# Kernel optimization log

Measured on AMD Instinct MI355X. Metric: run time of the kernel, lower is better.

Reference implementation:

```python
import jax, jax.numpy as jnp
import numpy as np

N_NODES = 1024
CHANNELS = [1, 64, 128]
DENSE = [196608, 256]
SAMPLE_NUMBER = 50


def _glorot(key, shape):
    fan_in, fan_out = shape[0], shape[-1]
    s = jnp.sqrt(6.0 / (fan_in + fan_out))
    return jax.random.uniform(key, shape, jnp.float32, -s, s)


def setup_inputs() -> dict:
    key = jax.random.key(0)
    ks = jax.random.split(key, 20)
    T, B = 16, 64
    inp = {
        "xs_seq": jax.random.normal(ks[0], (T, B, N_NODES, CHANNELS[0]), jnp.float32),
        "adj": jax.random.uniform(ks[1], (N_NODES, N_NODES), jnp.float32) / N_NODES,
    }
    # GCGRU params per layer: gates z, r, candidate n over concat([x, h])
    ki = 2
    for li in range(len(CHANNELS) - 1):
        cin, cout = CHANNELS[li], CHANNELS[li + 1]
        for g in ("z", "r", "n"):
            inp[f"W{g}{li}"] = _glorot(ks[ki], (cin + cout, cout)); ki += 1
            inp[f"b{g}{li}"] = jnp.zeros((cout,), jnp.float32)
    inp["W_mu"] = _glorot(ks[ki], (DENSE[0], DENSE[1])); ki += 1
    inp["b_mu"] = jnp.zeros((DENSE[1],), jnp.float32)
    inp["W_lv"] = _glorot(ks[ki], (DENSE[0], DENSE[1])); ki += 1
    inp["b_lv"] = jnp.zeros((DENSE[1],), jnp.float32)
    return inp


def _gcgru(xs, adj, Wz, bz, Wr, br, Wn, bn, cout):
    # xs: [T, B, N, cin]; graph-conv GRU over time via scan
    T, B, N, _ = xs.shape
    h0 = jnp.zeros((B, N, cout), xs.dtype)

    def gconv(a, x, W, b):  # adj @ x @ W + b
        return jnp.einsum("ij,bjc,cd->bid", a, x, W) + b

    def step(h, x):
        xh = jnp.concatenate([x, h], axis=-1)
        z = jax.nn.sigmoid(gconv(adj, xh, Wz, bz))
        r = jax.nn.sigmoid(gconv(adj, xh, Wr, br))
        xrh = jnp.concatenate([x, r * h], axis=-1)
        n = jnp.tanh(gconv(adj, xrh, Wn, bn))
        h_new = (1.0 - z) * h + z * n
        return h_new, h_new

    _, hs = jax.lax.scan(step, h0, xs)
    return hs  # [T, B, N, cout]


def _forward(xs_seq, adj, Wz0, bz0, Wr0, br0, Wn0, bn0,
             Wz1, bz1, Wr1, br1, Wn1, bn1, W_mu, b_mu, W_lv, b_lv, eps):
    h1 = _gcgru(xs_seq, adj, Wz0, bz0, Wr0, br0, Wn0, bn0, CHANNELS[1])
    h2 = _gcgru(h1, adj, Wz1, bz1, Wr1, br1, Wn1, bn1, CHANNELS[2])
    xs = jnp.concatenate([h1[-1], h2[-1]], axis=2)  # [B, N, C1+C2]
    B = xs.shape[0]
    xs = xs.reshape(B, -1)  # [B, N*(C1+C2)]
    mu = jax.nn.sigmoid(xs @ W_mu + b_mu)
    logvar = jax.nn.sigmoid(xs @ W_lv + b_lv)
    std = jnp.exp(0.5 * logvar)
    z = mu + eps * std
    return z, mu, logvar


def reference(xs_seq, adj, Wz0, bz0, Wr0, br0, Wn0, bn0,
              Wz1, bz1, Wr1, br1, Wn1, bn1, W_mu, b_mu, W_lv, b_lv):
    B = xs_seq.shape[1]
    ekey = jax.random.fold_in(jax.random.key(0), 1234)
    eps = jax.random.normal(ekey, (SAMPLE_NUMBER, B, DENSE[1]), jnp.float32).mean(0)
    return _forward(xs_seq, adj, Wz0, bz0, Wr0, br0, Wn0, bn0,
                    Wz1, bz1, Wr1, br1, Wn1, bn1, W_mu, b_mu, W_lv, b_lv, eps)
```

## Files before the change

kernel.cpp:

```cpp
#include <hip/hip_runtime.h>
#include <math.h>

#define EPS_MODE 0

typedef unsigned short u16;
typedef short bf16x8 __attribute__((ext_vector_type(8)));
typedef float f32x4 __attribute__((ext_vector_type(4)));
typedef u16 u16x4 __attribute__((ext_vector_type(4)));
typedef u16 u16x8 __attribute__((ext_vector_type(8)));

static constexpr int T = 16;
static constexpr size_t MF = 1u << 20;

__device__ __forceinline__ u16 f2bf(float f) {
  unsigned u = __float_as_uint(f);
  unsigned r = (u + 0x7fffu + ((u >> 16) & 1u)) >> 16;
  return (u16)r;
}
__device__ __forceinline__ float bf2f(u16 h) {
  return __uint_as_float(((unsigned)h) << 16);
}
__device__ __forceinline__ void gload16(const void* g, void* l) {
  __builtin_amdgcn_global_load_lds(
      (const __attribute__((address_space(1))) void*)g,
      (__attribute__((address_space(3))) void*)l, 16, 0, 0);
}

__global__ __launch_bounds__(256) void cast_bf16(const float* __restrict__ in,
                                                 u16* __restrict__ out, int n) {
  int i = (blockIdx.x * 256 + threadIdx.x) * 4;
  if (i < n) {
    float4 v = *reinterpret_cast<const float4*>(&in[i]);
    out[i + 0] = f2bf(v.x); out[i + 1] = f2bf(v.y);
    out[i + 2] = f2bf(v.z); out[i + 3] = f2bf(v.w);
  }
}

__global__ __launch_bounds__(256) void prep_wt(const float* __restrict__ Wz0, const float* __restrict__ Wr0,
                                               const float* __restrict__ Wn0, const float* __restrict__ Wz1,
                                               const float* __restrict__ Wr1, const float* __restrict__ Wn1,
                                               u16* __restrict__ WzrT0, u16* __restrict__ WnT0,
                                               u16* __restrict__ WzrT1, u16* __restrict__ WnT1) {
  int seg = blockIdx.y;
  int idx = blockIdx.x * 256 + threadIdx.x;
  if (seg == 0) {
    if (idx < 128 * 64) {
      int j = idx >> 6, k = idx & 63;
      float v = (j < 64) ? Wz0[(k + 1) * 64 + j] : Wr0[(k + 1) * 64 + (j - 64)];
      WzrT0[idx] = f2bf(v);
    }
  } else if (seg == 1) {
    if (idx < 64 * 64) {
      int j = idx >> 6, k = idx & 63;
      WnT0[idx] = f2bf(Wn0[(k + 1) * 64 + j]);
    }
  } else if (seg == 2) {
    if (idx < 256 * 192) {
      int j = idx / 192, k = idx % 192;
      float v = (j < 128) ? Wz1[k * 128 + j] : Wr1[k * 128 + (j - 128)];
      WzrT1[idx] = f2bf(v);
    }
  } else {
    if (idx < 128 * 192) {
      int j = idx / 192, k = idx % 192;
      WnT1[idx] = f2bf(Wn1[k * 128 + j]);
    }
  }
}

template <int EPI, int LOGC>
__global__ __launch_bounds__(256) void adj_mfma(const u16* __restrict__ A,
                                                const u16* __restrict__ BT,
                                                void* __restrict__ OUT) {
  __shared__ __align__(16) char lds[32768];
  int tid = threadIdx.x;
  int w = tid >> 6, lane = tid & 63;
  int row0 = blockIdx.y * 128, col0 = blockIdx.x * 128;
  int wm = w >> 1, wn = w & 1;
  f32x4 acc[4][4] = {};
  for (int k0 = 0; k0 < 1024; k0 += 64) {
#pragma unroll
    for (int q = 0; q < 4; ++q) {
      int row = q * 32 + w * 8 + (lane >> 3);
      gload16(A + (size_t)(row0 + row) * 1024 + k0 + (lane & 7) * 8,
              lds + q * 4096 + w * 1024);
    }
#pragma unroll
    for (int q = 0; q < 4; ++q) {
      int row = q * 32 + w * 8 + (lane >> 3);
      gload16(BT + (size_t)(col0 + row) * 1024 + k0 + (lane & 7) * 8,
              lds + 16384 + q * 4096 + w * 1024);
    }
    __syncthreads();
#pragma unroll
    for (int kk = 0; kk < 2; ++kk) {
      bf16x8 a[4], bb[4];
#pragma unroll
      for (int m = 0; m < 4; ++m)
        a[m] = *(const bf16x8*)(lds + (wm * 64 + m * 16 + (lane & 15)) * 128 + kk * 64 + (lane >> 4) * 16);
#pragma unroll
      for (int n = 0; n < 4; ++n)
        bb[n] = *(const bf16x8*)(lds + 16384 + (wn * 64 + n * 16 + (lane & 15)) * 128 + kk * 64 + (lane >> 4) * 16);
#pragma unroll
      for (int m = 0; m < 4; ++m)
#pragma unroll
        for (int n = 0; n < 4; ++n)
          acc[m][n] = __builtin_amdgcn_mfma_f32_16x16x32_bf16(a[m], bb[n], acc[m][n], 0, 0, 0);
    }
    __syncthreads();
  }
  if (EPI == 1) {
    float* O = (float*)OUT;
#pragma unroll
    for (int m = 0; m < 4; ++m)
#pragma unroll
      for (int n = 0; n < 4; ++n) {
        int col = col0 + wn * 64 + n * 16 + (lane & 15);
        int t = col >> 6, bbx = col & 63;
        int row = row0 + wm * 64 + m * 16 + ((lane >> 4) << 2);
        *(float4*)&O[((size_t)t << 16) + ((size_t)bbx << 10) + row] = *(float4*)&acc[m][n];
      }
  } else {
    u16* O = (u16*)OUT;
    constexpr int C = 1 << LOGC;
#pragma unroll
    for (int m = 0; m < 4; ++m)
#pragma unroll
      for (int n = 0; n < 4; ++n) {
        int col = col0 + wn * 64 + n * 16 + (lane & 15);
        int bbx = col >> LOGC, c = col & (C - 1);
#pragma unroll
        for (int j = 0; j < 4; ++j) {
          int row = row0 + wm * 64 + m * 16 + ((lane >> 4) << 2) + j;
          O[(((size_t)bbx << 10) + row) * C + c] = f2bf(acc[m][n][j]);
        }
      }
  }
}

template <int C, int RK1>
__global__ __launch_bounds__(256) void adj_ngate(
    const u16* __restrict__ A, const u16* __restrict__ BT,
    const u16* __restrict__ WnT, const float* __restrict__ bias,
    const float* __restrict__ axv, const float* __restrict__ wx,
    const u16* __restrict__ AH1, const u16* __restrict__ zT,
    u16* __restrict__ hT) {
  constexpr int LOGC = (C == 64) ? 6 : 7;
  constexpr int KW = (C == 64) ? 64 : 192;
  constexpr int KKAN = C / 32;
  __shared__ __align__(16) char lds[136 * 128 * 2];
  int tid = threadIdx.x;
  int w = tid >> 6, lane = tid & 63;
  int row0 = blockIdx.y * 128, col0 = blockIdx.x * 128;
  int wm = w >> 1, wn = w & 1;
  f32x4 acc[4][4] = {};
  for (int k0 = 0; k0 < 1024; k0 += 64) {
#pragma unroll
    for (int q = 0; q < 4; ++q) {
      int row = q * 32 + w * 8 + (lane >> 3);
      gload16(A + (size_t)(row0 + row) * 1024 + k0 + (lane & 7) * 8,
              lds + q * 4096 + w * 1024);
    }
#pragma unroll
    for (int q = 0; q < 4; ++q) {
      int row = q * 32 + w * 8 + (lane >> 3);
      gload16(BT + (size_t)(col0 + row) * 1024 + k0 + (lane & 7) * 8,
              lds + 16384 + q * 4096 + w * 1024);
    }
    __syncthreads();
#pragma unroll
    for (int kk = 0; kk < 2; ++kk) {
      bf16x8 a[4], bb[4];
#pragma unroll
      for (int m = 0; m < 4; ++m)
        a[m] = *(const bf16x8*)(lds + (wm * 64 + m * 16 + (lane & 15)) * 128 + kk * 64 + (lane >> 4) * 16);
#pragma unroll
      for (int n = 0; n < 4; ++n)
        bb[n] = *(const bf16x8*)(lds + 16384 + (wn * 64 + n * 16 + (lane & 15)) * 128 + kk * 64 + (lane >> 4) * 16);
#pragma unroll
      for (int m = 0; m < 4; ++m)
#pragma unroll
        for (int n = 0; n < 4; ++n)
          acc[m][n] = __builtin_amdgcn_mfma_f32_16x16x32_bf16(a[m], bb[n], acc[m][n], 0, 0, 0);
    }
    __syncthreads();
  }
  u16* ANt = (u16*)lds;
#pragma unroll
  for (int m = 0; m < 4; ++m)
#pragma unroll
    for (int n = 0; n < 4; ++n) {
      int cl = wn * 64 + n * 16 + (lane & 15);
      int rl = wm * 64 + m * 16 + ((lane >> 4) << 2);
#pragma unroll
      for (int j = 0; j < 4; ++j)
        ANt[(rl + j) * 136 + cl] = f2bf(acc[m][n][j]);
    }
  __syncthreads();
  int arow0 = (w >> 1) * 64;
  int half = w & 1;
  int b0 = col0 >> LOGC;
  int out0 = (C == 64) ? 0 : half * 64;
  int kbase = (C == 64) ? half * 64 : 0;
  int b_eff = (C == 64) ? (b0 + half) : b0;
  constexpr int WOFF = (C == 64) ? 0 : 64;
  f32x4 acc2[4][4] = {};
#pragma unroll
  for (int kk = 0; kk < KKAN; ++kk) {
    bf16x8 a[4], bb[4];
    int ka = kbase + kk * 32 + (lane >> 4) * 8;
#pragma unroll
    for (int m = 0; m < 4; ++m)
      a[m] = *(const bf16x8*)&ANt[(arow0 + m * 16 + (lane & 15)) * 136 + ka];
#pragma unroll
    for (int n = 0; n < 4; ++n)
      bb[n] = *(const bf16x8*)&WnT[(size_t)(out0 + n * 16 + (lane & 15)) * KW + WOFF + kk * 32 + (lane >> 4) * 8];
#pragma unroll
    for (int m = 0; m < 4; ++m)
#pragma unroll
      for (int n = 0; n < 4; ++n)
        acc2[m][n] = __builtin_amdgcn_mfma_f32_16x16x32_bf16(a[m], bb[n], acc2[m][n], 0, 0, 0);
  }
  if (C == 128) {
#pragma unroll
    for (int kk = 0; kk < 2; ++kk) {
      bf16x8 a[4], bb[4];
#pragma unroll
      for (int m = 0; m < 4; ++m)
        a[m] = *(const bf16x8*)&AH1[(((size_t)b0 << 10) + row0 + arow0 + m * 16 + (lane & 15)) * 64 + kk * 32 + (lane >> 4) * 8];
#pragma unroll
      for (int n = 0; n < 4; ++n)
        bb[n] = *(const bf16x8*)&WnT[(size_t)(out0 + n * 16 + (lane & 15)) * 192 + kk * 32 + (lane >> 4) * 8];
#pragma unroll
      for (int m = 0; m < 4; ++m)
#pragma unroll
        for (int n = 0; n < 4; ++n)
          acc2[m][n] = __builtin_amdgcn_mfma_f32_16x16x32_bf16(a[m], bb[n], acc2[m][n], 0, 0, 0);
    }
  }
#pragma unroll
  for (int m = 0; m < 4; ++m) {
    float ax4[4];
    if (RK1) {
      float4 v = *(const float4*)&axv[((size_t)b_eff << 10) + row0 + arow0 + m * 16 + ((lane >> 4) << 2)];
      ax4[0] = v.x; ax4[1] = v.y; ax4[2] = v.z; ax4[3] = v.w;
    }
#pragma unroll
    for (int n = 0; n < 4; ++n) {
      int cp = out0 + n * 16 + (lane & 15);
      int grow = arow0 + m * 16 + ((lane >> 4) << 2);
      size_t idx = (((size_t)b_eff << LOGC) + cp) * 1024 + row0 + grow;
      u16x4 zv = *(const u16x4*)&zT[idx];
      u16x4 hv = *(const u16x4*)&hT[idx];
      u16x4 pk;
#pragma unroll
      for (int j = 0; j < 4; ++j) {
        float g = acc2[m][n][j] + bias[cp];
        if (RK1) g += ax4[j] * wx[cp];
        float nv = tanhf(g);
        float z = bf2f(zv[j]), ho = bf2f(hv[j]);
        pk[j] = f2bf((1.f - z) * ho + z * nv);
      }
      *(u16x4*)&hT[idx] = pk;
    }
  }
}

template <int WM, int WN, int C, int NK1, int NK, int RK1>
__global__ __launch_bounds__(256) void gate_zr(
    const u16* __restrict__ A1, const u16* __restrict__ A2,
    const u16* __restrict__ WT, const float* __restrict__ bz,
    const float* __restrict__ br, const float* __restrict__ axv,
    const float* __restrict__ wxz, const float* __restrict__ wxr,
    const u16* __restrict__ hT, u16* __restrict__ zTo, u16* __restrict__ rhTo) {
  constexpr int MT = WM * 64, NT = WN * 64, K = NK * 64;
  constexpr int NB = 1024 / MT;
  __shared__ __align__(16) char lds[MT * 128 + NT * 128];
  int tid = threadIdx.x;
  int w = tid >> 6, lane = tid & 63;
  int by = blockIdx.x;
  int b = by / NB, n0 = (by % NB) * MT;
  size_t row0 = ((size_t)b << 10) + n0;
  int wm = w / WN, wn = w % WN;
  f32x4 acc[4][4] = {};
  for (int s = 0; s < NK; ++s) {
    const u16* As; int astr, koff;
    if (s < NK1) { As = A1; astr = 64; koff = s * 64; }
    else         { As = A2; astr = 128; koff = (s - NK1) * 64; }
#pragma unroll
    for (int q = 0; q < MT / 32; ++q) {
      int row = q * 32 + w * 8 + (lane >> 3);
      gload16(As + (row0 + row) * astr + koff + (lane & 7) * 8,
              lds + q * 4096 + w * 1024);
    }
#pragma unroll
    for (int q = 0; q < NT / 32; ++q) {
      int row = q * 32 + w * 8 + (lane >> 3);
      gload16(WT + (size_t)row * K + s * 64 + (lane & 7) * 8,
              lds + MT * 128 + q * 4096 + w * 1024);
    }
    __syncthreads();
#pragma unroll
    for (int kk = 0; kk < 2; ++kk) {
      bf16x8 a[4], bb[4];
#pragma unroll
      for (int m = 0; m < 4; ++m)
        a[m] = *(const bf16x8*)(lds + (wm * 64 + m * 16 + (lane & 15)) * 128 + kk * 64 + (lane >> 4) * 16);
#pragma unroll
      for (int n = 0; n < 4; ++n)
        bb[n] = *(const bf16x8*)(lds + MT * 128 + (wn * 64 + n * 16 + (lane & 15)) * 128 + kk * 64 + (lane >> 4) * 16);
#pragma unroll
      for (int m = 0; m < 4; ++m)
#pragma unroll
        for (int n = 0; n < 4; ++n)
          acc[m][n] = __builtin_amdgcn_mfma_f32_16x16x32_bf16(a[m], bb[n], acc[m][n], 0, 0, 0);
    }
    __syncthreads();
  }
#pragma unroll
  for (int m = 0; m < 4; ++m) {
    float ax4[4];
    if (RK1) {
      float4 v = *(const float4*)&axv[row0 + wm * 64 + m * 16 + ((lane >> 4) << 2)];
      ax4[0] = v.x; ax4[1] = v.y; ax4[2] = v.z; ax4[3] = v.w;
    }
#pragma unroll
    for (int n = 0; n < 4; ++n) {
      int cp = wn * 64 + n * 16 + (lane & 15);
      bool iz = cp < C;
      int c = iz ? cp : cp - C;
      int rl = wm * 64 + m * 16 + ((lane >> 4) << 2);
      size_t idx = (((size_t)b * C + c) << 10) + n0 + rl;
      u16x4 hv;
      if (!iz) hv = *(const u16x4*)&hT[idx];
      u16x4 pk;
#pragma unroll
      for (int j = 0; j < 4; ++j) {
        float g = acc[m][n][j] + (iz ? bz : br)[c];
        if (RK1) g += ax4[j] * (iz ? wxz : wxr)[c];
        float sg = 1.f / (1.f + expf(-g));
        pk[j] = iz ? f2bf(sg) : f2bf(sg * bf2f(hv[j]));
      }
      *(u16x4*)&(iz ? zTo : rhTo)[idx] = pk;
    }
  }
}

__global__ __launch_bounds__(256) void dense_gemm(const u16* __restrict__ h1T,
                                                  const u16* __restrict__ h2T,
                                                  const float* __restrict__ Wmu,
                                                  const float* __restrict__ Wlv,
                                                  float* __restrict__ P) {
  int ch = blockIdx.x, mat = blockIdx.y;
  const float* W = mat ? Wlv : Wmu;
  __shared__ float As[64][36];
  __shared__ float Ws[32][260];
  int tid = threadIdx.x;
  int k0 = ch * 512;
  bool is1 = ch < 128;
  const u16* hs = is1 ? h1T : h2T;
  int kloc = is1 ? k0 : (k0 - 65536);
  int bstr = is1 ? 65536 : 131072;
  int wofs = is1 ? 0 : 64;
  int ab = tid >> 2, aks = (tid & 3) * 8;
  int wkk = tid >> 3, woq = (tid & 7) * 32;
  int tx = tid & 15, ty = tid >> 4;
  float acc[4][16] = {};
  u16x8 av;
  float4 wv[8];
  int ka = kloc;
  av = *(const u16x8*)&hs[(size_t)ab * bstr + ka + aks];
  {
    int kw = ka + wkk;
    int nn = kw & 1023, cc = kw >> 10;
    const float* wp = &W[((size_t)nn * 192 + wofs + cc) * 256 + woq];
#pragma unroll
    for (int i = 0; i < 8; ++i) wv[i] = *(const float4*)(wp + i * 4);
  }
  for (int kit = 0; kit < 16; ++kit) {
    float4 f0, f1;
    f0.x = bf2f(av[0]); f0.y = bf2f(av[1]); f0.z = bf2f(av[2]); f0.w = bf2f(av[3]);
    f1.x = bf2f(av[4]); f1.y = bf2f(av[5]); f1.z = bf2f(av[6]); f1.w = bf2f(av[7]);
    *(float4*)&As[ab][aks] = f0;
    *(float4*)&As[ab][aks + 4] = f1;
#pragma unroll
    for (int i = 0; i < 8; ++i) *(float4*)&Ws[wkk][woq + i * 4] = wv[i];
    __syncthreads();
    if (kit + 1 < 16) {
      ka = kloc + (kit + 1) * 32;
      av = *(const u16x8*)&hs[(size_t)ab * bstr + ka + aks];
      int kw = ka + wkk;
      int nn = kw & 1023, cc = kw >> 10;
      const float* wp = &W[((size_t)nn * 192 + wofs + cc) * 256 + woq];
#pragma unroll
      for (int i = 0; i < 8; ++i) wv[i] = *(const float4*)(wp + i * 4);
    }
#pragma unroll
    for (int kk = 0; kk < 32; ++kk) {
      float a[4];
      a[0] = As[ty * 4 + 0][kk]; a[1] = As[ty * 4 + 1][kk];
      a[2] = As[ty * 4 + 2][kk]; a[3] = As[ty * 4 + 3][kk];
#pragma unroll
      for (int q = 0; q < 4; ++q) {
        float bb[4];
        *(float4*)bb = *(const float4*)&Ws[kk][q * 64 + tx * 4];
#pragma unroll
        for (int i = 0; i < 4; ++i)
#pragma unroll
          for (int j = 0; j < 4; ++j) acc[i][q * 4 + j] += a[i] * bb[j];
      }
    }
    __syncthreads();
  }
#pragma unroll
  for (int i = 0; i < 4; ++i)
#pragma unroll
    for (int q = 0; q < 4; ++q) {
      float4 v;
      v.x = acc[i][q * 4 + 0]; v.y = acc[i][q * 4 + 1];
      v.z = acc[i][q * 4 + 2]; v.w = acc[i][q * 4 + 3];
      *(float4*)&P[(((size_t)mat * 384 + ch) * 64 + ty * 4 + i) * 256 + q * 64 + tx * 4] = v;
    }
}

__device__ __forceinline__ unsigned rotl32(unsigned v, int s) {
  return (v << s) | (v >> (32 - s));
}
__device__ void threefry(unsigned k0, unsigned k1, unsigned x0, unsigned x1,
                         unsigned& o0, unsigned& o1) {
  unsigned ks2 = k0 ^ k1 ^ 0x1BD11BDAu;
  unsigned a = x0 + k0, b = x1 + k1;
#define TF_RND(rot) { a += b; b = rotl32(b, rot); b ^= a; }
  TF_RND(13) TF_RND(15) TF_RND(26) TF_RND(6)
  a += k1; b += ks2 + 1u;
  TF_RND(17) TF_RND(29) TF_RND(16) TF_RND(24)
  a += ks2; b += k0 + 2u;
  TF_RND(13) TF_RND(15) TF_RND(26) TF_RND(6)
  a += k0; b += k1 + 3u;
  TF_RND(17) TF_RND(29) TF_RND(16) TF_RND(24)
  a += k1; b += ks2 + 4u;
  TF_RND(13) TF_RND(15) TF_RND(26) TF_RND(6)
  a += ks2; b += k0 + 5u;
#undef TF_RND
  o0 = a; o1 = b;
}

__device__ float u32_to_normal(unsigned bits) {
  unsigned fb = (bits >> 9) | 0x3F800000u;
  float f = __uint_as_float(fb) - 1.0f;
  const float lo = -0.99999994f;
  float u = f * 2.0f + lo;
  u = fmaxf(lo, u);
  float w = -log1pf(-u * u);
  float p;
  if (w < 5.0f) {
    w -= 2.5f;
    p = 2.81022636e-08f;
    p = fmaf(p, w, 3.43273939e-07f);
    p = fmaf(p, w, -3.5233877e-06f);
    p = fmaf(p, w, -4.39150654e-06f);
    p = fmaf(p, w, 0.00021858087f);
    p = fmaf(p, w, -0.00125372503f);
    p = fmaf(p, w, -0.00417768164f);
    p = fmaf(p, w, 0.246640727f);
    p = fmaf(p, w, 1.50140941f);
  } else {
    w = sqrtf(w) - 3.0f;
    p = -0.000200214257f;
    p = fmaf(p, w, 0.000100950558f);
    p = fmaf(p, w, 0.00134934322f);
    p = fmaf(p, w, -0.00367342844f);
    p = fmaf(p, w, 0.00573950773f);
    p = fmaf(p, w, -0.0076224613f);
    p = fmaf(p, w, 0.00943887047f);
    p = fmaf(p, w, 1.00167406f);
    p = fmaf(p, w, 2.83297682f);
  }
  return 1.41421354f * (p * u);
}

__global__ __launch_bounds__(256) void eps_kernel(float* __restrict__ eps) {
  int b = blockIdx.x;
  int o = threadIdx.x;
  unsigned k0, k1;
  threefry(0u, 0u, 0u, 1234u, k0, k1);
  float s = 0.f;
  for (int smp = 0; smp < 50; ++smp) {
    unsigned idx = ((unsigned)smp * 64u + (unsigned)b) * 256u + (unsigned)o;
    unsigned o0, o1, bits;
#if EPS_MODE == 0
    threefry(k0, k1, 0u, idx, o0, o1);
    bits = o0 ^ o1;
#else
    unsigned pp = idx % 409600u, half = idx / 409600u;
    threefry(k0, k1, pp, pp + 409600u, o0, o1);
    bits = half ? o1 : o0;
#endif
    s += u32_to_normal(bits);
  }
  eps[b * 256 + o] = s / 50.0f;
}

__global__ __launch_bounds__(256) void final_kernel(const float* __restrict__ P,
                                                    const float* __restrict__ bmu,
                                                    const float* __restrict__ blv,
                                                    const float* __restrict__ eps,
                                                    float* __restrict__ out) {
  int b = blockIdx.x, o = threadIdx.x;
  float smu = 0.f, slv = 0.f;
  for (int ch = 0; ch < 384; ++ch) {
    smu += P[(((size_t)0 * 384 + ch) * 64 + b) * 256 + o];
    slv += P[(((size_t)1 * 384 + ch) * 64 + b) * 256 + o];
  }
  float mu = 1.f / (1.f + expf(-(smu + bmu[o])));
  float lv = 1.f / (1.f + expf(-(slv + blv[o])));
  float z = mu + eps[b * 256 + o] * expf(0.5f * lv);
  out[b * 256 + o] = z;
  out[16384 + b * 256 + o] = mu;
  out[32768 + b * 256 + o] = lv;
}

extern "C" void kernel_launch(void* const* d_in, const int* in_sizes, int n_in,
                              void* d_out, int out_size, void* d_ws, size_t ws_size,
                              hipStream_t stream) {
  (void)in_sizes; (void)n_in; (void)out_size; (void)ws_size;
  const float* xs  = (const float*)d_in[0];
  const float* adj = (const float*)d_in[1];
  const float* Wz0 = (const float*)d_in[2];  const float* bz0 = (const float*)d_in[3];
  const float* Wr0 = (const float*)d_in[4];  const float* br0 = (const float*)d_in[5];
  const float* Wn0 = (const float*)d_in[6];  const float* bn0 = (const float*)d_in[7];
  const float* Wz1 = (const float*)d_in[8];  const float* bz1 = (const float*)d_in[9];
  const float* Wr1 = (const float*)d_in[10]; const float* br1 = (const float*)d_in[11];
  const float* Wn1 = (const float*)d_in[12]; const float* bn1 = (const float*)d_in[13];
  const float* Wmu = (const float*)d_in[14]; const float* bmu = (const float*)d_in[15];
  const float* Wlv = (const float*)d_in[16]; const float* blv = (const float*)d_in[17];

  float* ws = (float*)d_ws;
  u16*  adjB  = (u16*)(ws);
  u16*  xsB   = (u16*)(ws + MF / 2);
  float* AXv  = ws + 1 * MF;
  u16*  h1T   = (u16*)(ws + 2 * MF);
  u16*  h2T   = (u16*)(ws + 4 * MF);
  u16*  z0T   = (u16*)(ws + 8 * MF);
  u16*  z1T   = (u16*)(ws + 10 * MF);
  u16*  rh0T  = (u16*)(ws + 14 * MF);
  u16*  rh1T  = (u16*)(ws + 16 * MF);
  u16*  AH1   = (u16*)(ws + 20 * MF);
  u16*  AH2   = (u16*)(ws + 22 * MF);
  u16*  WTb   = (u16*)(ws + 26 * MF);
  float* P    = ws + 26 * MF + MF / 4;
  float* EPS  = ws + 39 * MF;

  u16* WzrT0 = WTb;
  u16* WnT0  = WTb + 8192;
  u16* WzrT1 = WTb + 12288;
  u16* WnT1  = WTb + 61440;

  hipMemsetAsync(ws + 2 * MF, 0, 6 * MF * sizeof(float), stream);
  hipMemsetAsync(ws + 20 * MF, 0, 6 * MF * sizeof(float), stream);

  cast_bf16<<<1024, 256, 0, stream>>>(adj, adjB, 1 << 20);
  cast_bf16<<<1024, 256, 0, stream>>>(xs, xsB, 1 << 20);
  prep_wt<<<dim3(192, 4), 256, 0, stream>>>(Wz0, Wr0, Wn0, Wz1, Wr1, Wn1,
                                            WzrT0, WnT0, WzrT1, WnT1);

  adj_mfma<1, 0><<<dim3(8, 8), 256, 0, stream>>>(adjB, xsB, AXv);

  for (int t = 0; t < T; ++t) {
    const float* AXt = AXv + (size_t)t * 65536;
    gate_zr<2, 2, 64, 1, 1, 1><<<512, 256, 0, stream>>>(
        AH1, nullptr, WzrT0, bz0, br0, AXt, Wz0, Wr0, h1T, z0T, rh0T);
    adj_ngate<64, 1><<<dim3(32, 8), 256, 0, stream>>>(
        adjB, rh0T, WnT0, bn0, AXt, Wn0, nullptr, z0T, h1T);
    adj_mfma<0, 6><<<dim3(32, 8), 256, 0, stream>>>(adjB, h1T, AH1);
    gate_zr<1, 4, 128, 1, 3, 0><<<1024, 256, 0, stream>>>(
        AH1, AH2, WzrT1, bz1, br1, nullptr, nullptr, nullptr, h2T, z1T, rh1T);
    adj_ngate<128, 0><<<dim3(64, 8), 256, 0, stream>>>(
        adjB, rh1T, WnT1, bn1, nullptr, nullptr, AH1, z1T, h2T);
    if (t + 1 < T)
      adj_mfma<0, 7><<<dim3(64, 8), 256, 0, stream>>>(adjB, h2T, AH2);
  }

  dense_gemm<<<dim3(384, 2), 256, 0, stream>>>(h1T, h2T, Wmu, Wlv, P);
  eps_kernel<<<64, 256, 0, stream>>>(EPS);
  final_kernel<<<64, 256, 0, stream>>>(P, bmu, blv, EPS, (float*)d_out);
}
```

Before: 3.304 ms.

## Shrink adj GEMM row tiles for layer-0 and restructure dense head with transposed input

Adds a row-tile template parameter to the adjacency MFMA kernels and uses 64-row tiles for the layer-0 recurrent GEMMs, doubling their grid to fill more compute units. The final dense projection is rebuilt: the hidden states are first transposed into a contiguous [B, N*C] bf16 buffer, then a split-K GEMM with 64-wide output tiles over 256 K-chunks runs, and the reduction loop is resized to match. This aims to raise parallelism and make weight reads coalesced, at the cost of an extra transpose pass and smaller per-block reuse. Workspace offsets are reassigned to reuse earlier buffers.

New measurement: 3.025 ms. 8.5% less time.

```diff
diff --git a/kernel.cpp b/kernel.cpp
--- a/kernel.cpp
+++ b/kernel.cpp
@@ -11,6 +11,8 @@
 
 static constexpr int T = 16;
 static constexpr size_t MF = 1u << 20;
+static constexpr int DKCH = 256;
+static constexpr int DKCHUNK = 196608 / DKCH;
 
 __device__ __forceinline__ u16 f2bf(float f) {
   unsigned u = __float_as_uint(f);
@@ -68,19 +70,20 @@
   }
 }
 
-template <int EPI, int LOGC>
+template <int EPI, int LOGC, int MFR>
 __global__ __launch_bounds__(256) void adj_mfma(const u16* __restrict__ A,
                                                 const u16* __restrict__ BT,
                                                 void* __restrict__ OUT) {
-  __shared__ __align__(16) char lds[32768];
+  constexpr int MT = MFR * 32;
+  __shared__ __align__(16) char lds[(MFR + 4) * 4096];
   int tid = threadIdx.x;
   int w = tid >> 6, lane = tid & 63;
-  int row0 = blockIdx.y * 128, col0 = blockIdx.x * 128;
+  int row0 = blockIdx.y * MT, col0 = blockIdx.x * 128;
   int wm = w >> 1, wn = w & 1;
-  f32x4 acc[4][4] = {};
+  f32x4 acc[MFR][4] = {};
   for (int k0 = 0; k0 < 1024; k0 += 64) {
 #pragma unroll
-    for (int q = 0; q < 4; ++q) {
+    for (int q = 0; q < MFR; ++q) {
       int row = q * 32 + w * 8 + (lane >> 3);
       gload16(A + (size_t)(row0 + row) * 1024 + k0 + (lane & 7) * 8,
               lds + q * 4096 + w * 1024);
@@ -89,20 +92,20 @@
     for (int q = 0; q < 4; ++q) {
       int row = q * 32 + w * 8 + (lane >> 3);
       gload16(BT + (size_t)(col0 + row) * 1024 + k0 + (lane & 7) * 8,
-              lds + 16384 + q * 4096 + w * 1024);
+              lds + MFR * 4096 + q * 4096 + w * 1024);
     }
     __syncthreads();
 #pragma unroll
     for (int kk = 0; kk < 2; ++kk) {
-      bf16x8 a[4], bb[4];
-#pragma unroll
-      for (int m = 0; m < 4; ++m)
-        a[m] = *(const bf16x8*)(lds + (wm * 64 + m * 16 + (lane & 15)) * 128 + kk * 64 + (lane >> 4) * 16);
+      bf16x8 a[MFR], bb[4];
+#pragma unroll
+      for (int m = 0; m < MFR; ++m)
+        a[m] = *(const bf16x8*)(lds + (wm * (MFR * 16) + m * 16 + (lane & 15)) * 128 + kk * 64 + (lane >> 4) * 16);
 #pragma unroll
       for (int n = 0; n < 4; ++n)
-        bb[n] = *(const bf16x8*)(lds + 16384 + (wn * 64 + n * 16 + (lane & 15)) * 128 + kk * 64 + (lane >> 4) * 16);
-#pragma unroll
-      for (int m = 0; m < 4; ++m)
+        bb[n] = *(const bf16x8*)(lds + MFR * 4096 + (wn * 64 + n * 16 + (lane & 15)) * 128 + kk * 64 + (lane >> 4) * 16);
+#pragma unroll
+      for (int m = 0; m < MFR; ++m)
 #pragma unroll
         for (int n = 0; n < 4; ++n)
           acc[m][n] = __builtin_amdgcn_mfma_f32_16x16x32_bf16(a[m], bb[n], acc[m][n], 0, 0, 0);
@@ -112,33 +115,33 @@
   if (EPI == 1) {
     float* O = (float*)OUT;
 #pragma unroll
-    for (int m = 0; m < 4; ++m)
+    for (int m = 0; m < MFR; ++m)
 #pragma unroll
       for (int n = 0; n < 4; ++n) {
         int col = col0 + wn * 64 + n * 16 + (lane & 15);
         int t = col >> 6, bbx = col & 63;
-        int row = row0 + wm * 64 + m * 16 + ((lane >> 4) << 2);
+        int row = row0 + wm * (MFR * 16) + m * 16 + ((lane >> 4) << 2);
         *(float4*)&O[((size_t)t << 16) + ((size_t)bbx << 10) + row] = *(float4*)&acc[m][n];
       }
   } else {
     u16* O = (u16*)OUT;
     constexpr int C = 1 << LOGC;
 #pragma unroll
-    for (int m = 0; m < 4; ++m)
+    for (int m = 0; m < MFR; ++m)
 #pragma unroll
       for (int n = 0; n < 4; ++n) {
         int col = col0 + wn * 64 + n * 16 + (lane & 15);
         int bbx = col >> LOGC, c = col & (C - 1);
 #pragma unroll
         for (int j = 0; j < 4; ++j) {
-          int row = row0 + wm * 64 + m * 16 + ((lane >> 4) << 2) + j;
+          int row = row0 + wm * (MFR * 16) + m * 16 + ((lane >> 4) << 2) + j;
           O[(((size_t)bbx << 10) + row) * C + c] = f2bf(acc[m][n][j]);
         }
       }
   }
 }
 
-template <int C, int RK1>
+template <int C, int RK1, int MFR>
 __global__ __launch_bounds__(256) void adj_ngate(
     const u16* __restrict__ A, const u16* __restrict__ BT,
     const u16* __restrict__ WnT, const float* __restrict__ bias,
@@ -148,15 +151,19 @@
   constexpr int LOGC = (C == 64) ? 6 : 7;
   constexpr int KW = (C == 64) ? 64 : 192;
   constexpr int KKAN = C / 32;
-  __shared__ __align__(16) char lds[136 * 128 * 2];
+  constexpr int MT = MFR * 32;
+  constexpr int STG = (MFR + 4) * 4096;
+  constexpr int ANBYTES = MT * 136 * 2;
+  constexpr int LDSZ = STG > ANBYTES ? STG : ANBYTES;
+  __shared__ __align__(16) char lds[LDSZ];
   int tid = threadIdx.x;
   int w = tid >> 6, lane = tid & 63;
-  int row0 = blockIdx.y * 128, col0 = blockIdx.x * 128;
+  int row0 = blockIdx.y * MT, col0 = blockIdx.x * 128;
   int wm = w >> 1, wn = w & 1;
-  f32x4 acc[4][4] = {};
+  f32x4 acc[MFR][4] = {};
   for (int k0 = 0; k0 < 1024; k0 += 64) {
 #pragma unroll
-    for (int q = 0; q < 4; ++q) {
+    for (int q = 0; q < MFR; ++q) {
       int row = q * 32 + w * 8 + (lane >> 3);
       gload16(A + (size_t)(row0 + row) * 1024 + k0 + (lane & 7) * 8,
               lds + q * 4096 + w * 1024);
@@ -165,20 +172,20 @@
     for (int q = 0; q < 4; ++q) {
       int row = q * 32 + w * 8 + (lane >> 3);
       gload16(BT + (size_t)(col0 + row) * 1024 + k0 + (lane & 7) * 8,
-              lds + 16384 + q * 4096 + w * 1024);
+              lds + MFR * 4096 + q * 4096 + w * 1024);
     }
     __syncthreads();
 #pragma unroll
     for (int kk = 0; kk < 2; ++kk) {
-      bf16x8 a[4], bb[4];
-#pragma unroll
-      for (int m = 0; m < 4; ++m)
-        a[m] = *(const bf16x8*)(lds + (wm * 64 + m * 16 + (lane & 15)) * 128 + kk * 64 + (lane >> 4) * 16);
+      bf16x8 a[MFR], bb[4];
+#pragma unroll
+      for (int m = 0; m < MFR; ++m)
+        a[m] = *(const bf16x8*)(lds + (wm * (MFR * 16) + m * 16 + (lane & 15)) * 128 + kk * 64 + (lane >> 4) * 16);
 #pragma unroll
       for (int n = 0; n < 4; ++n)
-        bb[n] = *(const bf16x8*)(lds + 16384 + (wn * 64 + n * 16 + (lane & 15)) * 128 + kk * 64 + (lane >> 4) * 16);
-#pragma unroll
-      for (int m = 0; m < 4; ++m)
+        bb[n] = *(const bf16x8*)(lds + MFR * 4096 + (wn * 64 + n * 16 + (lane & 15)) * 128 + kk * 64 + (lane >> 4) * 16);
+#pragma unroll
+      for (int m = 0; m < MFR; ++m)
 #pragma unroll
         for (int n = 0; n < 4; ++n)
           acc[m][n] = __builtin_amdgcn_mfma_f32_16x16x32_bf16(a[m], bb[n], acc[m][n], 0, 0, 0);
@@ -187,36 +194,36 @@
   }
   u16* ANt = (u16*)lds;
 #pragma unroll
-  for (int m = 0; m < 4; ++m)
+  for (int m = 0; m < MFR; ++m)
 #pragma unroll
     for (int n = 0; n < 4; ++n) {
       int cl = wn * 64 + n * 16 + (lane & 15);
-      int rl = wm * 64 + m * 16 + ((lane >> 4) << 2);
+      int rl = wm * (MFR * 16) + m * 16 + ((lane >> 4) << 2);
 #pragma unroll
       for (int j = 0; j < 4; ++j)
         ANt[(rl + j) * 136 + cl] = f2bf(acc[m][n][j]);
     }
   __syncthreads();
-  int arow0 = (w >> 1) * 64;
-  int half = w & 1;
+  int wrow = w >> 1, half = w & 1;
+  int arow0 = wrow * (MFR * 16);
   int b0 = col0 >> LOGC;
   int out0 = (C == 64) ? 0 : half * 64;
   int kbase = (C == 64) ? half * 64 : 0;
   int b_eff = (C == 64) ? (b0 + half) : b0;
   constexpr int WOFF = (C == 64) ? 0 : 64;
-  f32x4 acc2[4][4] = {};
+  f32x4 acc2[MFR][4] = {};
 #pragma unroll
   for (int kk = 0; kk < KKAN; ++kk) {
-    bf16x8 a[4], bb[4];
+    bf16x8 a[MFR], bb[4];
     int ka = kbase + kk * 32 + (lane >> 4) * 8;
 #pragma unroll
-    for (int m = 0; m < 4; ++m)
+    for (int m = 0; m < MFR; ++m)
       a[m] = *(const bf16x8*)&ANt[(arow0 + m * 16 + (lane & 15)) * 136 + ka];
 #pragma unroll
     for (int n = 0; n < 4; ++n)
       bb[n] = *(const bf16x8*)&WnT[(size_t)(out0 + n * 16 + (lane & 15)) * KW + WOFF + kk * 32 + (lane >> 4) * 8];
 #pragma unroll
-    for (int m = 0; m < 4; ++m)
+    for (int m = 0; m < MFR; ++m)
 #pragma unroll
       for (int n = 0; n < 4; ++n)
         acc2[m][n] = __builtin_amdgcn_mfma_f32_16x16x32_bf16(a[m], bb[n], acc2[m][n], 0, 0, 0);
@@ -224,22 +231,22 @@
   if (C == 128) {
 #pragma unroll
     for (int kk = 0; kk < 2; ++kk) {
-      bf16x8 a[4], bb[4];
-#pragma unroll
-      for (int m = 0; m < 4; ++m)
+      bf16x8 a[MFR], bb[4];
+#pragma unroll
+      for (int m = 0; m < MFR; ++m)
         a[m] = *(const bf16x8*)&AH1[(((size_t)b0 << 10) + row0 + arow0 + m * 16 + (lane & 15)) * 64 + kk * 32 + (lane >> 4) * 8];
 #pragma unroll
       for (int n = 0; n < 4; ++n)
         bb[n] = *(const bf16x8*)&WnT[(size_t)(out0 + n * 16 + (lane & 15)) * 192 + kk * 32 + (lane >> 4) * 8];
 #pragma unroll
-      for (int m = 0; m < 4; ++m)
+      for (int m = 0; m < MFR; ++m)
 #pragma unroll
         for (int n = 0; n < 4; ++n)
           acc2[m][n] = __builtin_amdgcn_mfma_f32_16x16x32_bf16(a[m], bb[n], acc2[m][n], 0, 0, 0);
     }
   }
 #pragma unroll
-  for (int m = 0; m < 4; ++m) {
+  for (int m = 0; m < MFR; ++m) {
     float ax4[4];
     if (RK1) {
       float4 v = *(const float4*)&axv[((size_t)b_eff << 10) + row0 + arow0 + m * 16 + ((lane >> 4) << 2)];
@@ -346,81 +353,78 @@
   }
 }
 
-__global__ __launch_bounds__(256) void dense_gemm(const u16* __restrict__ h1T,
-                                                  const u16* __restrict__ h2T,
-                                                  const float* __restrict__ Wmu,
-                                                  const float* __restrict__ Wlv,
-                                                  float* __restrict__ P) {
-  int ch = blockIdx.x, mat = blockIdx.y;
+__global__ __launch_bounds__(256) void transpose_x(const u16* __restrict__ h1T,
+                                                   const u16* __restrict__ h2T,
+                                                   u16* __restrict__ X) {
+  int b = blockIdx.x;
+  int n0 = blockIdx.y * 128;
+  __shared__ u16 tile[192][136];
+  int tid = threadIdx.x;
+#pragma unroll
+  for (int i = 0; i < 12; ++i) {
+    int id = tid + i * 256;
+    int c = id >> 4, g = id & 15;
+    u16x8 v;
+    if (c < 64) v = *(const u16x8*)&h1T[(((size_t)b << 6) + c) * 1024 + n0 + g * 8];
+    else        v = *(const u16x8*)&h2T[(((size_t)b << 7) + (c - 64)) * 1024 + n0 + g * 8];
+    *(u16x8*)&tile[c][g * 8] = v;
+  }
+  __syncthreads();
+#pragma unroll
+  for (int i = 0; i < 12; ++i) {
+    int id = tid + i * 256;
+    int n = id / 24, g = id % 24;
+    u16x8 v;
+#pragma unroll
+    for (int j = 0; j < 8; ++j) v[j] = tile[g * 8 + j][n];
+    *(u16x8*)&X[(size_t)b * 196608 + (size_t)(n0 + n) * 192 + g * 8] = v;
+  }
+}
+
+__global__ __launch_bounds__(256) void dense_split(const u16* __restrict__ X,
+                                                   const float* __restrict__ Wmu,
+                                                   const float* __restrict__ Wlv,
+                                                   float* __restrict__ P) {
+  int ot = blockIdx.x, ch = blockIdx.y, mat = blockIdx.z;
   const float* W = mat ? Wlv : Wmu;
-  __shared__ float As[64][36];
-  __shared__ float Ws[32][260];
+  int o0 = ot * 64;
+  __shared__ float As[16][68];
+  __shared__ float Ws[16][68];
   int tid = threadIdx.x;
-  int k0 = ch * 512;
-  bool is1 = ch < 128;
-  const u16* hs = is1 ? h1T : h2T;
-  int kloc = is1 ? k0 : (k0 - 65536);
-  int bstr = is1 ? 65536 : 131072;
-  int wofs = is1 ? 0 : 64;
-  int ab = tid >> 2, aks = (tid & 3) * 8;
-  int wkk = tid >> 3, woq = (tid & 7) * 32;
   int tx = tid & 15, ty = tid >> 4;
-  float acc[4][16] = {};
-  u16x8 av;
-  float4 wv[8];
-  int ka = kloc;
-  av = *(const u16x8*)&hs[(size_t)ab * bstr + ka + aks];
-  {
-    int kw = ka + wkk;
-    int nn = kw & 1023, cc = kw >> 10;
-    const float* wp = &W[((size_t)nn * 192 + wofs + cc) * 256 + woq];
-#pragma unroll
-    for (int i = 0; i < 8; ++i) wv[i] = *(const float4*)(wp + i * 4);
-  }
-  for (int kit = 0; kit < 16; ++kit) {
-    float4 f0, f1;
-    f0.x = bf2f(av[0]); f0.y = bf2f(av[1]); f0.z = bf2f(av[2]); f0.w = bf2f(av[3]);
-    f1.x = bf2f(av[4]); f1.y = bf2f(av[5]); f1.z = bf2f(av[6]); f1.w = bf2f(av[7]);
-    *(float4*)&As[ab][aks] = f0;
-    *(float4*)&As[ab][aks + 4] = f1;
-#pragma unroll
-    for (int i = 0; i < 8; ++i) *(float4*)&Ws[wkk][woq + i * 4] = wv[i];
-    __syncthreads();
-    if (kit + 1 < 16) {
-      ka = kloc + (kit + 1) * 32;
-      av = *(const u16x8*)&hs[(size_t)ab * bstr + ka + aks];
-      int kw = ka + wkk;
-      int nn = kw & 1023, cc = kw >> 10;
-      const float* wp = &W[((size_t)nn * 192 + wofs + cc) * 256 + woq];
-#pragma unroll
-      for (int i = 0; i < 8; ++i) wv[i] = *(const float4*)(wp + i * 4);
-    }
-#pragma unroll
-    for (int kk = 0; kk < 32; ++kk) {
-      float a[4];
-      a[0] = As[ty * 4 + 0][kk]; a[1] = As[ty * 4 + 1][kk];
-      a[2] = As[ty * 4 + 2][kk]; a[3] = As[ty * 4 + 3][kk];
-#pragma unroll
-      for (int q = 0; q < 4; ++q) {
-        float bb[4];
-        *(float4*)bb = *(const float4*)&Ws[kk][q * 64 + tx * 4];
-#pragma unroll
-        for (int i = 0; i < 4; ++i)
-#pragma unroll
-          for (int j = 0; j < 4; ++j) acc[i][q * 4 + j] += a[i] * bb[j];
-      }
-    }
-    __syncthreads();
-  }
-#pragma unroll
-  for (int i = 0; i < 4; ++i)
-#pragma unroll
-    for (int q = 0; q < 4; ++q) {
-      float4 v;
-      v.x = acc[i][q * 4 + 0]; v.y = acc[i][q * 4 + 1];
-      v.z = acc[i][q * 4 + 2]; v.w = acc[i][q * 4 + 3];
-      *(float4*)&P[(((size_t)mat * 384 + ch) * 64 + ty * 4 + i) * 256 + q * 64 + tx * 4] = v;
-    }
+  int ab = tid >> 2, akq = (tid & 3) * 4;
+  int wkk = tid >> 4, wo4 = (tid & 15) * 4;
+  int kb = ch * DKCHUNK;
+  float acc[4][4] = {};
+  u16x4 xa = *(const u16x4*)&X[(size_t)ab * 196608 + kb + akq];
+  float4 wv = *(const float4*)&W[(size_t)(kb + wkk) * 256 + o0 + wo4];
+  for (int s = 0; s < DKCHUNK / 16; ++s) {
+#pragma unroll
+    for (int j = 0; j < 4; ++j) As[akq + j][ab] = bf2f(xa[j]);
+    *(float4*)&Ws[wkk][wo4] = wv;
+    __syncthreads();
+    if (s + 1 < DKCHUNK / 16) {
+      int k0 = kb + (s + 1) * 16;
+      xa = *(const u16x4*)&X[(size_t)ab * 196608 + k0 + akq];
+      wv = *(const float4*)&W[(size_t)(k0 + wkk) * 256 + o0 + wo4];
+    }
+#pragma unroll
+    for (int kk = 0; kk < 16; ++kk) {
+      float a[4], bq[4];
+      *(float4*)a = *(const float4*)&As[kk][ty * 4];
+      *(float4*)bq = *(const float4*)&Ws[kk][tx * 4];
+#pragma unroll
+      for (int i = 0; i < 4; ++i)
+#pragma unroll
+        for (int j = 0; j < 4; ++j) acc[i][j] += a[i] * bq[j];
+    }
+    __syncthreads();
+  }
+#pragma unroll
+  for (int i = 0; i < 4; ++i) {
+    float4 v; v.x = acc[i][0]; v.y = acc[i][1]; v.z = acc[i][2]; v.w = acc[i][3];
+    *(float4*)&P[(((size_t)mat * DKCH + ch) * 64 + ty * 4 + i) * 256 + o0 + tx * 4] = v;
+  }
 }
 
 __device__ __forceinline__ unsigned rotl32(unsigned v, int s) {
@@ -508,9 +512,9 @@
                                                     float* __restrict__ out) {
   int b = blockIdx.x, o = threadIdx.x;
   float smu = 0.f, slv = 0.f;
-  for (int ch = 0; ch < 384; ++ch) {
-    smu += P[(((size_t)0 * 384 + ch) * 64 + b) * 256 + o];
-    slv += P[(((size_t)1 * 384 + ch) * 64 + b) * 256 + o];
+  for (int ch = 0; ch < DKCH; ++ch) {
+    smu += P[(((size_t)0 * DKCH + ch) * 64 + b) * 256 + o];
+    slv += P[(((size_t)1 * DKCH + ch) * 64 + b) * 256 + o];
   }
   float mu = 1.f / (1.f + expf(-(smu + bmu[o])));
   float lv = 1.f / (1.f + expf(-(slv + blv[o])));
@@ -548,8 +552,9 @@
   u16*  AH1   = (u16*)(ws + 20 * MF);
   u16*  AH2   = (u16*)(ws + 22 * MF);
   u16*  WTb   = (u16*)(ws + 26 * MF);
-  float* P    = ws + 26 * MF + MF / 4;
-  float* EPS  = ws + 39 * MF;
+  u16*  X     = (u16*)(ws + 8 * MF);
+  float* P    = ws + 16 * MF;
+  float* EPS  = ws + 24 * MF;
 
   u16* WzrT0 = WTb;
   u16* WnT0  = WTb + 8192;
@@ -564,24 +569,25 @@
   prep_wt<<<dim3(192, 4), 256, 0, stream>>>(Wz0, Wr0, Wn0, Wz1, Wr1, Wn1,
                                             WzrT0, WnT0, WzrT1, WnT1);
 
-  adj_mfma<1, 0><<<dim3(8, 8), 256, 0, stream>>>(adjB, xsB, AXv);
+  adj_mfma<1, 0, 4><<<dim3(8, 8), 256, 0, stream>>>(adjB, xsB, AXv);
 
   for (int t = 0; t < T; ++t) {
     const float* AXt = AXv + (size_t)t * 65536;
     gate_zr<2, 2, 64, 1, 1, 1><<<512, 256, 0, stream>>>(
         AH1, nullptr, WzrT0, bz0, br0, AXt, Wz0, Wr0, h1T, z0T, rh0T);
-    adj_ngate<64, 1><<<dim3(32, 8), 256, 0, stream>>>(
+    adj_ngate<64, 1, 2><<<dim3(32, 16), 256, 0, stream>>>(
         adjB, rh0T, WnT0, bn0, AXt, Wn0, nullptr, z0T, h1T);
-    adj_mfma<0, 6><<<dim3(32, 8), 256, 0, stream>>>(adjB, h1T, AH1);
+    adj_mfma<0, 6, 2><<<dim3(32, 16), 256, 0, stream>>>(adjB, h1T, AH1);
     gate_zr<1, 4, 128, 1, 3, 0><<<1024, 256, 0, stream>>>(
         AH1, AH2, WzrT1, bz1, br1, nullptr, nullptr, nullptr, h2T, z1T, rh1T);
-    adj_ngate<128, 0><<<dim3(64, 8), 256, 0, stream>>>(
+    adj_ngate<128, 0, 4><<<dim3(64, 8), 256, 0, stream>>>(
         adjB, rh1T, WnT1, bn1, nullptr, nullptr, AH1, z1T, h2T);
     if (t + 1 < T)
-      adj_mfma<0, 7><<<dim3(64, 8), 256, 0, stream>>>(adjB, h2T, AH2);
-  }
-
-  dense_gemm<<<dim3(384, 2), 256, 0, stream>>>(h1T, h2T, Wmu, Wlv, P);
+      adj_mfma<0, 7, 4><<<dim3(64, 8), 256, 0, stream>>>(adjB, h2T, AH2);
+  }
+
+  transpose_x<<<dim3(64, 8), 256, 0, stream>>>(h1T, h2T, X);
+  dense_split<<<dim3(4, DKCH, 2), 256, 0, stream>>>(X, Wmu, Wlv, P);
   eps_kernel<<<64, 256, 0, stream>>>(EPS);
   final_kernel<<<64, 256, 0, stream>>>(P, bmu, blv, EPS, (float*)d_out);
 }
```
